# Performance work log

Measured on AMD Instinct MI355X. Metric: run time of the kernel, lower is better.

The kernel has to match this reference:

```python
import jax, jax.numpy as jnp
import numpy as np

HID, INP, BATCH, TIME = 1024, 512, 128, 256


def _kaiming(key, d1, d2, gain):
    # kaiming_normal_: std = gain / sqrt(fan_in), fan_in = d2
    return jax.random.normal(key, (d1, d2), jnp.float32) * (gain / np.sqrt(d2))


def setup_inputs() -> dict:
    key = jax.random.key(0)
    ks = jax.random.split(key, 9)
    g_lin = 1.0          # nonlinearity='linear'
    g_tanh = 5.0 / 3.0   # nonlinearity='tanh'
    inp = {
        "x": jax.random.normal(ks[0], (BATCH, TIME, INP), jnp.float32),
        "c": jnp.zeros((HID, BATCH), jnp.float32),
        "h": jnp.zeros((HID, BATCH), jnp.float32),
        "W_gx": _kaiming(ks[1], HID, INP, g_lin),
        "W_ix": _kaiming(ks[2], HID, INP, g_lin),
        "W_fx": _kaiming(ks[3], HID, INP, g_lin),
        "W_ox": _kaiming(ks[4], HID, INP, g_lin),
        "W_gh": _kaiming(ks[5], HID, HID, g_tanh),
        "W_ih": _kaiming(ks[6], HID, HID, g_tanh),
        "W_fh": _kaiming(ks[7], HID, HID, g_tanh),
        "W_oh": _kaiming(ks[8], HID, HID, g_tanh),
        "b_g": jnp.zeros((HID, 1), jnp.float32),
        "b_i": jnp.zeros((HID, 1), jnp.float32),
        "b_f": jnp.zeros((HID, 1), jnp.float32),
        "b_o": jnp.zeros((HID, 1), jnp.float32),
    }
    return inp


def reference(x, c, h, W_gx, W_ix, W_fx, W_ox, W_gh, W_ih, W_fh, W_oh,
              b_g, b_i, b_f, b_o):
    Hd = W_gx.shape[0]
    # Fuse the four gate GEMMs into one: same math, single contraction.
    Wx = jnp.concatenate([W_gx, W_ix, W_fx, W_ox], axis=0)   # (4H, I)
    Wh = jnp.concatenate([W_gh, W_ih, W_fh, W_oh], axis=0)   # (4H, H)
    b = jnp.concatenate([b_g, b_i, b_f, b_o], axis=0)[:, 0]  # (4H,)
    # Precompute all input projections: (T, B, 4H)
    xs = jnp.einsum('bti,gi->tbg', x, Wx)

    def step(carry, xt):
        c_t, h_t = carry                      # (B, H)
        z = xt + h_t @ Wh.T + b               # (B, 4H)
        g = jnp.tanh(z[:, :Hd])
        i = jax.nn.sigmoid(z[:, Hd:2 * Hd])
        f = jax.nn.sigmoid(z[:, 2 * Hd:3 * Hd])
        o = jax.nn.sigmoid(z[:, 3 * Hd:])
        c_n = g * i + c_t * f
        h_n = jnp.tanh(c_n) * o
        return (c_n, h_n), None

    (c_f, h_f), _ = jax.lax.scan(step, (c.T, h.T), xs)
    return h_f.T  # (H, B), matching the torch layout
```

## Files before the change

### kernel.cpp

```cpp
#include <hip/hip_runtime.h>
#include <cstdint>
#include <cstddef>

#define HID 1024
#define INP 512
#define BATCH 128
#define TSTEPS 256
#define NK16 96
#define HSLOTS 32
#define NBLK_CHUNK 256
#define HSLOT ((size_t)64 * 4 * 2 * 512)

using short8  = __attribute__((ext_vector_type(8))) short;
using f32x16  = __attribute__((ext_vector_type(16))) float;

#define LD8(p) (*(const short8*)(p))
#define MFMA32(a,b,c) __builtin_amdgcn_mfma_f32_32x32x16_bf16((a),(b),(c),0,0,0)

static __device__ __forceinline__ unsigned short f2bf(float f) {
    union { float f; unsigned int u; } v; v.f = f;
    unsigned int r = v.u + 0x7fffu + ((v.u >> 16) & 1u);
    return (unsigned short)(r >> 16);
}
static __device__ __forceinline__ float bf2f(unsigned short b) {
    union { unsigned int u; float f; } v; v.u = ((unsigned int)b) << 16;
    return v.f;
}
static __device__ __forceinline__ float sigmoid_f(float z) {
    return 1.0f / (1.0f + __expf(-z));
}
static __device__ __forceinline__ float tanh_f(float z) {
    return 2.0f / (1.0f + __expf(-2.0f * z)) - 1.0f;
}


__global__ void prep_w(const float* __restrict__ Wgx, const float* __restrict__ Wix,
                       const float* __restrict__ Wfx, const float* __restrict__ Wox,
                       const float* __restrict__ Wgh, const float* __restrict__ Wih,
                       const float* __restrict__ Wfh, const float* __restrict__ Woh,
                       unsigned short* __restrict__ wfrag)
{
    const int k16 = blockIdx.x;
    const int s   = blockIdx.y;
    const int tid  = threadIdx.x;
    const int lane = tid >> 2;
    const int e0   = (tid & 3) * 2;
    const int row  = s * 32 + (lane & 31);
    const int k    = k16 * 16 + (lane >> 5) * 8 + e0;
    const int j = row >> 2;
    const int g = row & 3;
    float f0, f1;
    if (k < INP) {
        const float* wx = (g == 0 ? Wgx : g == 1 ? Wix : g == 2 ? Wfx : Wox) + (size_t)j * INP;
        f0 = wx[k]; f1 = wx[k + 1];
    } else {
        const float* wh = (g == 0 ? Wgh : g == 1 ? Wih : g == 2 ? Wfh : Woh) + (size_t)j * HID;
        f0 = wh[k - INP]; f1 = wh[k - INP + 1];
    }
    ushort2 hi, lo;
    hi.x = f2bf(f0); lo.x = f2bf(f0 - bf2f(hi.x));
    hi.y = f2bf(f1); lo.y = f2bf(f1 - bf2f(hi.y));
    unsigned short* base = wfrag + ((size_t)(s * NK16 + k16) * 2) * 512 + lane * 8 + e0;
    *(ushort2*)(base)       = hi;
    *(ushort2*)(base + 512) = lo;
}

__global__ void prep_x(const float* __restrict__ x, unsigned short* __restrict__ xfrag)
{
    const int k16x = blockIdx.x;
    const int t    = blockIdx.y;
    const int tid  = threadIdx.x;
    const int cg   = tid >> 6;
    const int lane = tid & 63;
    const int col  = cg * 32 + (lane & 31);
    const int k0   = k16x * 16 + (lane >> 5) * 8;
    const float* src = x + ((size_t)col * TSTEPS + t) * INP + k0;
    const float4 v0 = *(const float4*)(src);
    const float4 v1 = *(const float4*)(src + 4);
    ushort4 h0, l0, h1, l1;
    h0.x = f2bf(v0.x); l0.x = f2bf(v0.x - bf2f(h0.x));
    h0.y = f2bf(v0.y); l0.y = f2bf(v0.y - bf2f(h0.y));
    h0.z = f2bf(v0.z); l0.z = f2bf(v0.z - bf2f(h0.z));
    h0.w = f2bf(v0.w); l0.w = f2bf(v0.w - bf2f(h0.w));
    h1.x = f2bf(v1.x); l1.x = f2bf(v1.x - bf2f(h1.x));
    h1.y = f2bf(v1.y); l1.y = f2bf(v1.y - bf2f(h1.y));
    h1.z = f2bf(v1.z); l1.z = f2bf(v1.z - bf2f(h1.z));
    h1.w = f2bf(v1.w); l1.w = f2bf(v1.w - bf2f(h1.w));
    unsigned short* base = xfrag +
        ((size_t)(((size_t)t * 32 + k16x) * 4 + cg) * 2) * 512 + lane * 8;
    *(ushort4*)(base)           = h0;
    *(ushort4*)(base + 4)       = h1;
    *(ushort4*)(base + 512)     = l0;
    *(ushort4*)(base + 512 + 4) = l1;
}

__global__ void prep_state(const float* __restrict__ cin, const float* __restrict__ hin,
                           float* __restrict__ cdst, unsigned short* __restrict__ hslot,
                           unsigned* __restrict__ flags)
{
    if (blockIdx.x == 0) flags[threadIdx.x] = 0u;
    const int idx = blockIdx.x * 256 + threadIdx.x;
    cdst[idx] = cin[idx];
    const int j = idx >> 7;
    const int b = idx & 127;
    float f = hin[idx];
    unsigned short hh = f2bf(f);
    unsigned short hl = f2bf(f - bf2f(hh));
    const int k16h = j >> 4;
    const int hlf  = (j >> 3) & 1;
    const int e    = j & 7;
    const int cg   = b >> 5;
    const int lane = 32 * hlf + (b & 31);
    unsigned short* base = hslot +
        ((size_t)((k16h * 4 + cg) * 2) * 512) + lane * 8 + e;
    base[0]   = hh;
    base[512] = hl;
}

__global__ __launch_bounds__(512, 2) void lstm_persist(
    const unsigned short* __restrict__ wfrag,
    const unsigned short* __restrict__ xfrag,
    unsigned short* __restrict__ hbuf,
    float* __restrict__ cst,
    const float* __restrict__ bg, const float* __restrict__ bi,
    const float* __restrict__ bf_, const float* __restrict__ bo,
    float* __restrict__ outf,
    unsigned* __restrict__ flags)
{
    const int tid  = threadIdx.x;
    const int wv   = tid >> 6;
    const int lane = tid & 63;
    const int l31  = lane & 31;
    const int hl   = lane >> 5;
    const int bx   = blockIdx.x;

    const int xcd     = bx & 7;
    const int ii      = bx >> 3;
    const int s       = xcd * 16 + (ii >> 1);
    const int cb      = ii & 1;
    const int colbase = cb << 6;

    const int ejl  = tid >> 6;
    const int ecl  = tid & 63;
    const int ej   = s * 8 + ejl;
    const int ecol = colbase + ecl;
    const size_t ci = (size_t)ej * BATCH + ecol;

    const float bias0 = bg[ej], bias1 = bi[ej], bias2 = bf_[ej], bias3 = bo[ej];
    float creg = cst[ci];

    const size_t bOff = (size_t)(4 * wv + 2 * cb) * 1024 + lane * 8;
    const int k16h = s >> 1;
    const int cgg   = (colbase >> 5) + (ecl >> 5);
    const int lane8 = 32 * (s & 1) + (ecl & 31);
    const size_t hscat = ((size_t)((k16h * 4 + cgg) * 2) * 512) + lane8 * 8 + ejl;

    __shared__ unsigned short WhLds[65536];
    __shared__ float part[3][32][64];

    {
        const unsigned short* src = wfrag + (size_t)(s * NK16 + 32) * 2 * 512;
#pragma unroll
        for (int c = 0; c < 16; ++c) {
            const int cid = c * 512 + tid;
            *(short8*)(WhLds + (size_t)cid * 8) = LD8(src + (size_t)cid * 8);
        }
    }
    short8 wxh[4], wxl[4];
    {
        const unsigned short* pWx = wfrag + ((size_t)(s * NK16 + wv) * 2) * 512 + lane * 8;
#pragma unroll
        for (int m = 0; m < 4; ++m) {
            wxh[m] = LD8(pWx);
            wxl[m] = LD8(pWx + 512);
            pWx += 8192;
        }
    }
    __syncthreads();

#pragma unroll 1
    for (int t = 0; t < TSTEPS; ++t) {
        f32x16 a0A, a0B, a1A, a1B;
#pragma unroll
        for (int r = 0; r < 16; ++r) { a0A[r]=0.f; a0B[r]=0.f; a1A[r]=0.f; a1B[r]=0.f; }

        {
            short8 xh0[4], xl0[4], xh1[4], xl1[4];
            const unsigned short* pX = xfrag + (size_t)t * 131072 + bOff;
#pragma unroll
            for (int m = 0; m < 4; ++m) {
                xh0[m] = LD8(pX);
                xl0[m] = LD8(pX + 512);
                xh1[m] = LD8(pX + 1024);
                xl1[m] = LD8(pX + 1536);
                pX += 32768;
            }
#pragma unroll
            for (int m = 0; m < 4; ++m) {
                a0A = MFMA32(wxh[m], xh0[m], a0A);
                a1A = MFMA32(wxh[m], xh1[m], a1A);
                a0B = MFMA32(wxh[m], xl0[m], a0B);
                a1B = MFMA32(wxh[m], xl1[m], a1B);
                a0A = MFMA32(wxl[m], xh0[m], a0A);
                a1A = MFMA32(wxl[m], xh1[m], a1A);
            }
        }

        if (t > 0) {
            const unsigned target = (unsigned)t;
            int done;
            int guard = 0;
            do {
                unsigned v = target;
                if (tid < 256)
                    v = __hip_atomic_load(&flags[tid], __ATOMIC_RELAXED,
                                          __HIP_MEMORY_SCOPE_AGENT);
                done = __syncthreads_count(v >= target);
                if (done < 512) __builtin_amdgcn_s_sleep(1);
            } while (done < 512 && ++guard < (1 << 20));
            asm volatile("" ::: "memory");
            __builtin_amdgcn_sched_barrier(0);
            if ((t & 31) == 0)
                __builtin_amdgcn_fence(__ATOMIC_ACQUIRE, "agent");
        }

        {
            const unsigned short* pH = hbuf
                + (size_t)((t + HSLOTS - 1) & (HSLOTS - 1)) * HSLOT + bOff;
            short8 bh0[3], bl0[3], bh1[3], bl1[3];
#pragma unroll
            for (int i = 0; i < 2; ++i) {
                bh0[i] = LD8(pH);
                bl0[i] = LD8(pH + 512);
                bh1[i] = LD8(pH + 1024);
                bl1[i] = LD8(pH + 1536);
                pH += 32768;
            }
#pragma unroll
            for (int m = 0; m < 8; ++m) {
                const int cur = m % 3;
                const int nxt = (m + 2) % 3;
                if (m < 6) {
                    bh0[nxt] = LD8(pH);
                    bl0[nxt] = LD8(pH + 512);
                    bh1[nxt] = LD8(pH + 1024);
                    bl1[nxt] = LD8(pH + 1536);
                    pH += 32768;
                }
                const unsigned short* wp = WhLds + (size_t)((8 * m + wv) * 2) * 512 + lane * 8;
                short8 Ah = *(const short8*)(wp);
                short8 Al = *(const short8*)(wp + 512);
                a0A = MFMA32(Ah, bh0[cur], a0A);
                a1A = MFMA32(Ah, bh1[cur], a1A);
                a0B = MFMA32(Ah, bl0[cur], a0B);
                a1B = MFMA32(Ah, bl1[cur], a1B);
                a0A = MFMA32(Al, bh0[cur], a0A);
                a1A = MFMA32(Al, bh1[cur], a1A);
            }
        }

        if (wv >= 5) {
#pragma unroll
            for (int r = 0; r < 16; ++r) {
                const int lr = (r & 3) + 8 * (r >> 2) + 4 * hl;
                part[wv - 5][lr][l31]      = a0A[r] + a0B[r];
                part[wv - 5][lr][32 + l31] = a1A[r] + a1B[r];
            }
        }
        __syncthreads();
        if (wv >= 2 && wv < 5) {
#pragma unroll
            for (int r = 0; r < 16; ++r) {
                const int lr = (r & 3) + 8 * (r >> 2) + 4 * hl;
                part[wv - 2][lr][l31]      += a0A[r] + a0B[r];
                part[wv - 2][lr][32 + l31] += a1A[r] + a1B[r];
            }
        }
        __syncthreads();
        if (wv < 2) {
#pragma unroll
            for (int r = 0; r < 16; ++r) {
                const int lr = (r & 3) + 8 * (r >> 2) + 4 * hl;
                part[wv][lr][l31]      += a0A[r] + a0B[r];
                part[wv][lr][32 + l31] += a1A[r] + a1B[r];
            }
        }
        __syncthreads();

        {
            unsigned short* hout = hbuf + (size_t)(t & (HSLOTS - 1)) * HSLOT;
            const int r0 = 4 * ejl;
            float z0g = bias0 + part[0][r0 + 0][ecl] + part[1][r0 + 0][ecl] + part[2][r0 + 0][ecl];
            float z1g = bias1 + part[0][r0 + 1][ecl] + part[1][r0 + 1][ecl] + part[2][r0 + 1][ecl];
            float z2g = bias2 + part[0][r0 + 2][ecl] + part[1][r0 + 2][ecl] + part[2][r0 + 2][ecl];
            float z3g = bias3 + part[0][r0 + 3][ecl] + part[1][r0 + 3][ecl] + part[2][r0 + 3][ecl];
            float gg = tanh_f(z0g);
            float ig = sigmoid_f(z1g);
            float fg = sigmoid_f(z2g);
            float og = sigmoid_f(z3g);
            float cn = gg * ig + creg * fg;
            creg = cn;
            float hh = tanh_f(cn) * og;
            unsigned short hb  = f2bf(hh);
            unsigned short hlo = f2bf(hh - bf2f(hb));
            __hip_atomic_store(hout + hscat, hb,
                               __ATOMIC_RELAXED, __HIP_MEMORY_SCOPE_AGENT);
            __hip_atomic_store(hout + hscat + 512, hlo,
                               __ATOMIC_RELAXED, __HIP_MEMORY_SCOPE_AGENT);
            if (outf && t == TSTEPS - 1) outf[ci] = hh;
        }

        asm volatile("s_waitcnt vmcnt(0)" ::: "memory");
        __syncthreads();
        if (tid == 0)
            __hip_atomic_store(&flags[bx], (unsigned)(t + 1),
                               __ATOMIC_RELAXED, __HIP_MEMORY_SCOPE_AGENT);
    }
    cst[ci] = creg;
}

__global__ __launch_bounds__(512, 1) void lstm_step(
    const unsigned short* __restrict__ wfrag,
    const unsigned short* __restrict__ xfrag,
    const unsigned short* __restrict__ hin,
    unsigned short* __restrict__ hout,
    float* __restrict__ cst,
    const float* __restrict__ bg, const float* __restrict__ bi,
    const float* __restrict__ bf_, const float* __restrict__ bo,
    float* __restrict__ outf, int t)
{
    const int tid  = threadIdx.x;
    const int wv   = tid >> 6;
    const int lane = tid & 63;
    const int l31  = lane & 31;
    const int hl   = lane >> 5;
    const int bx   = blockIdx.x;

    const int xcd     = bx & 7;
    const int ii      = bx >> 3;
    const int s       = xcd * 16 + (ii >> 1);
    const int cb      = ii & 1;
    const int colbase = cb << 6;

    const int ejl  = tid >> 6;
    const int ecl  = tid & 63;
    const int ej   = s * 8 + ejl;
    const int ecol = colbase + ecl;

    float add0 = bg[ej], add1 = bi[ej], add2 = bf_[ej], add3 = bo[ej];
    const size_t ci = (size_t)ej * BATCH + ecol;
    float cold = cst[ci];

    f32x16 a0A, a0B, a1A, a1B;
#pragma unroll
    for (int r = 0; r < 16; ++r) { a0A[r]=0.f; a0B[r]=0.f; a1A[r]=0.f; a1B[r]=0.f; }

    const size_t bOff = (size_t)(4 * wv + 2 * cb) * 1024 + lane * 8;

    {
        const unsigned short* pA = wfrag + ((size_t)(s * NK16 + wv) * 2) * 512 + lane * 8;
        const unsigned short* pX = xfrag + (size_t)t * 131072 + bOff;
#pragma unroll
        for (int m = 0; m < 4; ++m) {
            short8 Ah  = LD8(pA);
            short8 Al  = LD8(pA + 512);
            short8 B0h = LD8(pX);
            short8 B0l = LD8(pX + 512);
            short8 B1h = LD8(pX + 1024);
            short8 B1l = LD8(pX + 1536);
            pA += 8192; pX += 32768;
            a0A = MFMA32(Ah, B0h, a0A);
            a1A = MFMA32(Ah, B1h, a1A);
            a0B = MFMA32(Ah, B0l, a0B);
            a1B = MFMA32(Ah, B1l, a1B);
            a0A = MFMA32(Al, B0h, a0A);
            a1A = MFMA32(Al, B1h, a1A);
        }
        const unsigned short* pH = hin + bOff;
#pragma unroll
        for (int m = 0; m < 8; ++m) {
            short8 Ah  = LD8(pA);
            short8 Al  = LD8(pA + 512);
            short8 B0h = LD8(pH);
            short8 B0l = LD8(pH + 512);
            short8 B1h = LD8(pH + 1024);
            short8 B1l = LD8(pH + 1536);
            pA += 8192; pH += 32768;
            a0A = MFMA32(Ah, B0h, a0A);
            a1A = MFMA32(Ah, B1h, a1A);
            a0B = MFMA32(Ah, B0l, a0B);
            a1B = MFMA32(Ah, B1l, a1B);
            a0A = MFMA32(Al, B0h, a0A);
            a1A = MFMA32(Al, B1h, a1A);
        }
    }

    __shared__ float part[8][32][64];
#pragma unroll
    for (int r = 0; r < 16; ++r) {
        const int lr = (r & 3) + 8 * (r >> 2) + 4 * hl;
        part[wv][lr][l31]      = a0A[r] + a0B[r];
        part[wv][lr][32 + l31] = a1A[r] + a1B[r];
    }
    __syncthreads();

    {
        const int r0 = 4 * ejl;
        float z0g = add0, z1g = add1, z2g = add2, z3g = add3;
#pragma unroll
        for (int p = 0; p < 8; ++p) {
            z0g += part[p][r0 + 0][ecl];
            z1g += part[p][r0 + 1][ecl];
            z2g += part[p][r0 + 2][ecl];
            z3g += part[p][r0 + 3][ecl];
        }
        float gg = tanh_f(z0g);
        float ig = sigmoid_f(z1g);
        float fg = sigmoid_f(z2g);
        float og = sigmoid_f(z3g);
        float cn = gg * ig + cold * fg;
        cst[ci] = cn;
        float hh = tanh_f(cn) * og;
        unsigned short hb  = f2bf(hh);
        unsigned short hlo = f2bf(hh - bf2f(hb));
        const int k16h  = s >> 1;
        const int cgg   = (colbase >> 5) + (ecl >> 5);
        const int lane8 = 32 * (s & 1) + (ecl & 31);
        unsigned short* dst = hout +
            ((size_t)((k16h * 4 + cgg) * 2) * 512) + lane8 * 8 + ejl;
        dst[0]   = hb;
        dst[512] = hlo;
        if (outf) outf[ci] = hh;
    }
}

extern "C" void kernel_launch(void* const* d_in, const int* in_sizes, int n_in,
                              void* d_out, int out_size, void* d_ws, size_t ws_size,
                              hipStream_t stream)
{
    const float* x   = (const float*)d_in[0];
    const float* c0v = (const float*)d_in[1];
    const float* h0v = (const float*)d_in[2];
    const float* Wgx = (const float*)d_in[3];
    const float* Wix = (const float*)d_in[4];
    const float* Wfx = (const float*)d_in[5];
    const float* Wox = (const float*)d_in[6];
    const float* Wgh = (const float*)d_in[7];
    const float* Wih = (const float*)d_in[8];
    const float* Wfh = (const float*)d_in[9];
    const float* Woh = (const float*)d_in[10];
    const float* bg  = (const float*)d_in[11];
    const float* bi  = (const float*)d_in[12];
    const float* bf  = (const float*)d_in[13];
    const float* bo  = (const float*)d_in[14];

    unsigned short* wfrag = (unsigned short*)d_ws;
    unsigned short* xfrag = wfrag + (size_t)128 * NK16 * 2 * 512;
    unsigned short* hbuf  = xfrag + (size_t)TSTEPS * 32 * 4 * 2 * 512;
    float* cst            = (float*)(hbuf + (size_t)HSLOTS * HSLOT);
    unsigned* flags       = (unsigned*)(cst + (size_t)HID * BATCH);

    const size_t needA = (size_t)((char*)(flags + 1024) - (char*)d_ws);
    const bool useA = (ws_size >= needA);

    float* outp = (float*)d_out;

    prep_w<<<dim3(NK16, 128), dim3(256), 0, stream>>>(Wgx, Wix, Wfx, Wox,
                                                      Wgh, Wih, Wfh, Woh, wfrag);
    prep_x<<<dim3(32, TSTEPS), dim3(256), 0, stream>>>(x, xfrag);
    prep_state<<<dim3(512), dim3(256), 0, stream>>>(c0v, h0v, cst,
                                                    hbuf + (size_t)(HSLOTS - 1) * HSLOT,
                                                    flags);

    bool done = false;
    if (useA) {
        const unsigned short* a_wfrag = wfrag;
        const unsigned short* a_xfrag = xfrag;
        unsigned short* a_hbuf = hbuf;
        float* a_cst = cst;
        const float* a_bg = bg; const float* a_bi = bi;
        const float* a_bf = bf; const float* a_bo = bo;
        float* a_out = outp;
        unsigned* a_flags = flags;
        void* kargs[] = { (void*)&a_wfrag, (void*)&a_xfrag, (void*)&a_hbuf,
                          (void*)&a_cst, (void*)&a_bg, (void*)&a_bi,
                          (void*)&a_bf, (void*)&a_bo, (void*)&a_out,
                          (void*)&a_flags };
        hipError_t ce = hipLaunchCooperativeKernel(
            (const void*)lstm_persist, dim3(NBLK_CHUNK), dim3(512),
            kargs, 0, stream);
        done = (ce == hipSuccess);
    }

    if (!done) {
        unsigned short* hfA = hbuf + (size_t)(HSLOTS - 1) * HSLOT;
        unsigned short* hfB = hbuf + (size_t)(HSLOTS - 2) * HSLOT;
        for (int t = 0; t < TSTEPS; ++t) {
            const unsigned short* hin = (t & 1) ? hfB : hfA;
            unsigned short* hout      = (t & 1) ? hfA : hfB;
            lstm_step<<<dim3(256), dim3(512), 0, stream>>>(
                wfrag, xfrag, hin, hout,
                cst, bg, bi, bf, bo,
                (t == TSTEPS - 1) ? outp : nullptr, t);
        }
    }
}
```

Before: 2.488 ms.

## Prefetch next-step x fragments, stage h stores in LDS, batch h loads

Measured after the change: 2.160 ms. 1.15x faster.

```diff
diff --git a/kernel.cpp b/kernel.cpp
--- a/kernel.cpp
+++ b/kernel.cpp
@@ -117,7 +117,7 @@
     base[512] = hl;
 }
 
-__global__ __launch_bounds__(512, 2) void lstm_persist(
+__global__ __launch_bounds__(512, 1) void lstm_persist(
     const unsigned short* __restrict__ wfrag,
     const unsigned short* __restrict__ xfrag,
     unsigned short* __restrict__ hbuf,
@@ -151,12 +151,11 @@
 
     const size_t bOff = (size_t)(4 * wv + 2 * cb) * 1024 + lane * 8;
     const int k16h = s >> 1;
-    const int cgg   = (colbase >> 5) + (ecl >> 5);
-    const int lane8 = 32 * (s & 1) + (ecl & 31);
-    const size_t hscat = ((size_t)((k16h * 4 + cgg) * 2) * 512) + lane8 * 8 + ejl;
 
     __shared__ unsigned short WhLds[65536];
     __shared__ float part[3][32][64];
+    __shared__ unsigned long long hstage[256];
+    unsigned short* hs16 = (unsigned short*)hstage;
 
     {
         const unsigned short* src = wfrag + (size_t)(s * NK16 + 32) * 2 * 512;
@@ -176,36 +175,22 @@
             pWx += 8192;
         }
     }
+    short8 xb0h[4], xb0l[4], xb1h[4], xb1l[4];
+    {
+        const unsigned short* pX = xfrag + bOff;
+#pragma unroll
+        for (int m = 0; m < 4; ++m) {
+            xb0h[m] = LD8(pX);
+            xb0l[m] = LD8(pX + 512);
+            xb1h[m] = LD8(pX + 1024);
+            xb1l[m] = LD8(pX + 1536);
+            pX += 32768;
+        }
+    }
     __syncthreads();
 
 #pragma unroll 1
     for (int t = 0; t < TSTEPS; ++t) {
-        f32x16 a0A, a0B, a1A, a1B;
-#pragma unroll
-        for (int r = 0; r < 16; ++r) { a0A[r]=0.f; a0B[r]=0.f; a1A[r]=0.f; a1B[r]=0.f; }
-
-        {
-            short8 xh0[4], xl0[4], xh1[4], xl1[4];
-            const unsigned short* pX = xfrag + (size_t)t * 131072 + bOff;
-#pragma unroll
-            for (int m = 0; m < 4; ++m) {
-                xh0[m] = LD8(pX);
-                xl0[m] = LD8(pX + 512);
-                xh1[m] = LD8(pX + 1024);
-                xl1[m] = LD8(pX + 1536);
-                pX += 32768;
-            }
-#pragma unroll
-            for (int m = 0; m < 4; ++m) {
-                a0A = MFMA32(wxh[m], xh0[m], a0A);
-                a1A = MFMA32(wxh[m], xh1[m], a1A);
-                a0B = MFMA32(wxh[m], xl0[m], a0B);
-                a1B = MFMA32(wxh[m], xl1[m], a1B);
-                a0A = MFMA32(wxl[m], xh0[m], a0A);
-                a1A = MFMA32(wxl[m], xh1[m], a1A);
-            }
-        }
-
         if (t > 0) {
             const unsigned target = (unsigned)t;
             int done;
@@ -224,39 +209,53 @@
                 __builtin_amdgcn_fence(__ATOMIC_ACQUIRE, "agent");
         }
 
-        {
-            const unsigned short* pH = hbuf
-                + (size_t)((t + HSLOTS - 1) & (HSLOTS - 1)) * HSLOT + bOff;
-            short8 bh0[3], bl0[3], bh1[3], bl1[3];
-#pragma unroll
-            for (int i = 0; i < 2; ++i) {
-                bh0[i] = LD8(pH);
-                bl0[i] = LD8(pH + 512);
-                bh1[i] = LD8(pH + 1024);
-                bl1[i] = LD8(pH + 1536);
-                pH += 32768;
-            }
-#pragma unroll
-            for (int m = 0; m < 8; ++m) {
-                const int cur = m % 3;
-                const int nxt = (m + 2) % 3;
-                if (m < 6) {
-                    bh0[nxt] = LD8(pH);
-                    bl0[nxt] = LD8(pH + 512);
-                    bh1[nxt] = LD8(pH + 1024);
-                    bl1[nxt] = LD8(pH + 1536);
-                    pH += 32768;
-                }
-                const unsigned short* wp = WhLds + (size_t)((8 * m + wv) * 2) * 512 + lane * 8;
-                short8 Ah = *(const short8*)(wp);
-                short8 Al = *(const short8*)(wp + 512);
-                a0A = MFMA32(Ah, bh0[cur], a0A);
-                a1A = MFMA32(Ah, bh1[cur], a1A);
-                a0B = MFMA32(Ah, bl0[cur], a0B);
-                a1B = MFMA32(Ah, bl1[cur], a1B);
-                a0A = MFMA32(Al, bh0[cur], a0A);
-                a1A = MFMA32(Al, bh1[cur], a1A);
-            }
+        f32x16 a0A, a0B, a1A, a1B;
+#pragma unroll
+        for (int r = 0; r < 16; ++r) { a0A[r]=0.f; a0B[r]=0.f; a1A[r]=0.f; a1B[r]=0.f; }
+
+        const unsigned short* pH = hbuf
+            + (size_t)((t + HSLOTS - 1) & (HSLOTS - 1)) * HSLOT + bOff;
+
+        short8 hb0h[8], hb0l[8], hb1h[8], hb1l[8];
+#pragma unroll
+        for (int m = 0; m < 4; ++m) {
+            hb0h[m] = LD8(pH);
+            hb0l[m] = LD8(pH + 512);
+            hb1h[m] = LD8(pH + 1024);
+            hb1l[m] = LD8(pH + 1536);
+            pH += 32768;
+        }
+
+#pragma unroll
+        for (int m = 0; m < 4; ++m) {
+            a0A = MFMA32(wxh[m], xb0h[m], a0A);
+            a1A = MFMA32(wxh[m], xb1h[m], a1A);
+            a0B = MFMA32(wxh[m], xb0l[m], a0B);
+            a1B = MFMA32(wxh[m], xb1l[m], a1B);
+            a0A = MFMA32(wxl[m], xb0h[m], a0A);
+            a1A = MFMA32(wxl[m], xb1h[m], a1A);
+        }
+
+#pragma unroll
+        for (int m = 4; m < 8; ++m) {
+            hb0h[m] = LD8(pH);
+            hb0l[m] = LD8(pH + 512);
+            hb1h[m] = LD8(pH + 1024);
+            hb1l[m] = LD8(pH + 1536);
+            pH += 32768;
+        }
+
+#pragma unroll
+        for (int m = 0; m < 8; ++m) {
+            const unsigned short* wp = WhLds + (size_t)((8 * m + wv) * 2) * 512 + lane * 8;
+            short8 Ah = *(const short8*)(wp);
+            short8 Al = *(const short8*)(wp + 512);
+            a0A = MFMA32(Ah, hb0h[m], a0A);
+            a1A = MFMA32(Ah, hb1h[m], a1A);
+            a0B = MFMA32(Ah, hb0l[m], a0B);
+            a1B = MFMA32(Ah, hb1l[m], a1B);
+            a0A = MFMA32(Al, hb0h[m], a0A);
+            a1A = MFMA32(Al, hb1h[m], a1A);
         }
 
         if (wv >= 5) {
@@ -288,7 +287,6 @@
         __syncthreads();
 
         {
-            unsigned short* hout = hbuf + (size_t)(t & (HSLOTS - 1)) * HSLOT;
             const int r0 = 4 * ejl;
             float z0g = bias0 + part[0][r0 + 0][ecl] + part[1][r0 + 0][ecl] + part[2][r0 + 0][ecl];
             float z1g = bias1 + part[0][r0 + 1][ecl] + part[1][r0 + 1][ecl] + part[2][r0 + 1][ecl];
@@ -303,18 +301,43 @@
             float hh = tanh_f(cn) * og;
             unsigned short hb  = f2bf(hh);
             unsigned short hlo = f2bf(hh - bf2f(hb));
-            __hip_atomic_store(hout + hscat, hb,
-                               __ATOMIC_RELAXED, __HIP_MEMORY_SCOPE_AGENT);
-            __hip_atomic_store(hout + hscat + 512, hlo,
-                               __ATOMIC_RELAXED, __HIP_MEMORY_SCOPE_AGENT);
+            hs16[((ecl >> 5) * 2 + 0) * 256 + (ecl & 31) * 8 + ejl] = hb;
+            hs16[((ecl >> 5) * 2 + 1) * 256 + (ecl & 31) * 8 + ejl] = hlo;
             if (outf && t == TSTEPS - 1) outf[ci] = hh;
         }
-
+        __syncthreads();
+
+        {
+            unsigned short* hout = hbuf + (size_t)(t & (HSLOTS - 1)) * HSLOT;
+            if (tid < 256) {
+                const int r   = tid >> 6;
+                const int w   = tid & 63;
+                const int cgg = 2 * cb + (r >> 1);
+                const int p   = r & 1;
+                const size_t uo = ((size_t)((k16h * 4 + cgg) * 2 + p)) * 512
+                                + 32 * (s & 1) * 8 + w * 4;
+                __hip_atomic_store((unsigned long long*)(hout + uo), hstage[tid],
+                                   __ATOMIC_RELAXED, __HIP_MEMORY_SCOPE_AGENT);
+            }
+        }
         asm volatile("s_waitcnt vmcnt(0)" ::: "memory");
         __syncthreads();
         if (tid == 0)
             __hip_atomic_store(&flags[bx], (unsigned)(t + 1),
                                __ATOMIC_RELAXED, __HIP_MEMORY_SCOPE_AGENT);
+
+        {
+            const int tn = (t + 1 < TSTEPS) ? (t + 1) : t;
+            const unsigned short* pX = xfrag + (size_t)tn * 131072 + bOff;
+#pragma unroll
+            for (int m = 0; m < 4; ++m) {
+                xb0h[m] = LD8(pX);
+                xb0l[m] = LD8(pX + 512);
+                xb1h[m] = LD8(pX + 1024);
+                xb1l[m] = LD8(pX + 1536);
+                pX += 32768;
+            }
+        }
     }
     cst[ci] = creg;
 }
```
